# Kernel tuning notes

Hardware: AMD Instinct MI355X
Metric: run time of the kernel (lower is better)

The kernel has to match this reference:

```python
import jax, jax.numpy as jnp
import numpy as np
import math

B, S, E, H = 2, 4096, 1024, 16
W = 256  # one-sided attention window (attention_window // 2)


def setup_inputs() -> dict:
    key = jax.random.key(0)
    ks = jax.random.split(key, 7)
    init = lambda k, shp: jax.random.normal(k, shp, jnp.float32) * 0.02
    return {
        "hidden_states": jax.random.normal(ks[0], (B, S, E), jnp.float32),
        "attention_mask": jnp.zeros((B, S), jnp.int32),  # 0 = local attention
        "q_w": init(ks[1], (E, E)), "q_b": jnp.zeros((E,), jnp.float32),
        "k_w": init(ks[2], (E, E)), "k_b": jnp.zeros((E,), jnp.float32),
        "v_w": init(ks[3], (E, E)), "v_b": jnp.zeros((E,), jnp.float32),
    }


def _banded_attention(hidden_states, attention_mask, q_w, q_b, k_w, k_b, v_w, v_b):
    D = E // H          # head dim
    w = W               # one-sided window
    nc = S // w         # number of query chunks of length w
    # Projections (torch Linear: x @ W.T + b); query pre-scaled by sqrt(head_dim)
    q = (hidden_states @ q_w.T + q_b) / math.sqrt(D)
    k = hidden_states @ k_w.T + k_b
    v = hidden_states @ v_w.T + v_b
    heads = lambda x: x.reshape(B, S, H, D).transpose(0, 2, 1, 3)  # [B,H,S,D]
    q, k, v = heads(q), heads(k), heads(v)

    qc = q.reshape(B, H, nc, w, D)                       # [B,H,nc,w,D]
    pad = lambda x: jnp.pad(x, ((0, 0), (0, 0), (w, w), (0, 0)))
    # chunk c of keys/values covers padded positions [c*w, c*w + 3w)
    idx = (jnp.arange(nc) * w)[:, None] + jnp.arange(3 * w)[None, :]  # [nc,3w]
    kc = pad(k)[:, :, idx]                               # [B,H,nc,3w,D]
    vc = pad(v)[:, :, idx]                               # [B,H,nc,3w,D]

    # banded scores: query x in chunk attends padded key y; rel offset = y-w-x
    scores = jnp.einsum('bhcxd,bhcyd->bhcxy', qc, kc)    # [B,H,nc,w,3w]

    # additive mask from attention_mask (!=0 -> -10000 at that key position)
    fm = jnp.where(attention_mask != 0, -10000.0, 0.0)   # [B,S]
    fmc = jnp.pad(fm, ((0, 0), (w, w)))[:, idx]          # [B,nc,3w]
    scores = scores + fmc[:, None, :, None, :]

    # validity: |rel| <= w (the 2w+1 band) and key index j in [0, S)
    x = jnp.arange(w)[:, None]                           # [w,1]
    y = jnp.arange(3 * w)[None, :]                       # [1,3w]
    rel = y - w - x                                      # [w,3w]
    j = (jnp.arange(nc) * w)[:, None, None] + (y - w)[None]  # [nc,1,3w] key idx
    valid = (jnp.abs(rel) <= w)[None] & (j >= 0) & (j < S)   # [nc,w,3w]
    scores = jnp.where(valid[None, None], scores, -jnp.inf)

    probs = jax.nn.softmax(scores.astype(jnp.float32), axis=-1)
    ctx = jnp.einsum('bhcxy,bhcyd->bhcxd', probs, vc)    # [B,H,nc,w,D]
    return ctx.reshape(B, H, S, D).transpose(0, 2, 1, 3).reshape(B, S, E)


def reference(hidden_states, attention_mask, q_w, q_b, k_w, k_b, v_w, v_b):
    return _banded_attention(hidden_states, attention_mask,
                             q_w, q_b, k_w, k_b, v_w, v_b)
```

## Files before the change

### kernel.cpp

```cpp
#include <hip/hip_runtime.h>
#include <math.h>

constexpr int Bn  = 2;
constexpr int Sn  = 4096;
constexpr int En  = 1024;
constexpr int Hn  = 16;
constexpr int Mtot = Bn * Sn;
constexpr int Kp  = 1024;
constexpr int QT   = 128;
constexpr int NST  = 10;
constexpr int PADK = 68;
constexpr int PADP = 36;

typedef __bf16    bf16x8 __attribute__((ext_vector_type(8)));
typedef __bf16    bf16x4 __attribute__((ext_vector_type(4)));
typedef _Float16  f16x8  __attribute__((ext_vector_type(8)));
typedef _Float16  f16x4  __attribute__((ext_vector_type(4)));
typedef float     f32x4  __attribute__((ext_vector_type(4)));

__global__ void __launch_bounds__(256)
cvt_all_kernel(const float* __restrict__ hs,
               const float* __restrict__ qw, const float* __restrict__ kw,
               const float* __restrict__ vw,
               _Float16* __restrict__ hs16, _Float16* __restrict__ w16)
{
    if (blockIdx.x < 8192) {
        int t = blockIdx.x * 256 + threadIdx.x;
        int m = t >> 8;
        int k = (t & 255) << 2;
        float4 x = *(const float4*)&hs[((size_t)m << 10) + k];
        f16x4 h;
        h[0] = (_Float16)x.x; h[1] = (_Float16)x.y;
        h[2] = (_Float16)x.z; h[3] = (_Float16)x.w;
        *(f16x4*)&hs16[((size_t)m << 10) + k] = h;
    } else {
        int t = (blockIdx.x - 8192) * 256 + threadIdx.x;
        int gn = t >> 8;
        int k  = (t & 255) << 2;
        int p  = gn >> 10, n = gn & 1023;
        const float* src = (p == 0) ? qw : (p == 1) ? kw : vw;
        float4 x = *(const float4*)&src[((size_t)n << 10) + k];
        f16x4 h;
        h[0] = (_Float16)x.x; h[1] = (_Float16)x.y;
        h[2] = (_Float16)x.z; h[3] = (_Float16)x.w;
        *(f16x4*)&w16[((size_t)gn << 10) + k] = h;
    }
}

__device__ inline void load_lds16(const void* g, void* s) {
    __builtin_amdgcn_global_load_lds((const __attribute__((address_space(1))) void*)g,
                                     (__attribute__((address_space(3))) void*)s,
                                     16, 0, 0);
}

__global__ void __launch_bounds__(256)
qkv_mfma_kernel(const _Float16* __restrict__ A2, const _Float16* __restrict__ B2,
                const float* __restrict__ qb, const float* __restrict__ kb,
                const float* __restrict__ vb,
                __bf16* __restrict__ q16, __bf16* __restrict__ k16,
                __bf16* __restrict__ vt16)
{
    __shared__ _Float16 As[128 * 32];
    __shared__ _Float16 Bs[128 * 32];

    const int tid  = threadIdx.x;
    const int m0   = blockIdx.x * 128;
    const int n0   = blockIdx.y * 128;
    const int w    = tid >> 6;
    const int lane = tid & 63;
    const int wm   = w >> 1, wn = w & 1;
    const int mrow = lane & 15, quad = lane >> 4;

    const int stRow = w * 16 + (lane >> 2);
    const int stCol = (lane & 3) * 8;

    f32x4 acc[4][4] = {};

    const _Float16* Abase = A2 + (size_t)(m0 + stRow) * Kp + stCol;
    const _Float16* Bbase = B2 + (size_t)(n0 + stRow) * Kp + stCol;
    _Float16* AsW = &As[w * 512];
    _Float16* BsW = &Bs[w * 512];

    for (int k0 = 0; k0 < Kp; k0 += 32) {
        load_lds16(Abase + k0,            AsW);
        load_lds16(Abase + 64 * Kp + k0,  AsW + 2048);
        load_lds16(Bbase + k0,            BsW);
        load_lds16(Bbase + 64 * Kp + k0,  BsW + 2048);
        __syncthreads();
        f16x8 af[4], bfr[4];
#pragma unroll
        for (int t = 0; t < 4; t++) {
            af[t]  = *(const f16x8*)&As[(wm * 64 + t * 16 + mrow) * 32 + quad * 8];
            bfr[t] = *(const f16x8*)&Bs[(wn * 64 + t * 16 + mrow) * 32 + quad * 8];
        }
#pragma unroll
        for (int ti = 0; ti < 4; ti++)
#pragma unroll
            for (int tj = 0; tj < 4; tj++)
                acc[ti][tj] = __builtin_amdgcn_mfma_f32_16x16x32_f16(
                    af[ti], bfr[tj], acc[ti][tj], 0, 0, 0);
        __syncthreads();
    }

    const int p = n0 >> 10;
    const float* bptr = (p == 0) ? qb : (p == 1) ? kb : vb;
#pragma unroll
    for (int tj = 0; tj < 4; tj++) {
        const int n  = n0 + wn * 64 + tj * 16 + mrow;
        const float bv = bptr[n & 1023];
        const int hh = (n & 1023) >> 6, dd = n & 63;
#pragma unroll
        for (int ti = 0; ti < 4; ti++) {
            const int m  = m0 + wm * 64 + ti * 16 + quad * 4;
            const int bb = m >> 12, ss = m & 4095;
            const size_t bhh = (size_t)(bb * Hn + hh);
            if (p == 0) {
#pragma unroll
                for (int r = 0; r < 4; r++)
                    q16[(bhh * Sn + ss + r) * 64 + dd] =
                        (__bf16)((acc[ti][tj][r] + bv) * 0.125f);
            } else if (p == 1) {
#pragma unroll
                for (int r = 0; r < 4; r++)
                    k16[(bhh * Sn + ss + r) * 64 + dd] =
                        (__bf16)(acc[ti][tj][r] + bv);
            } else {
                bf16x4 pv4;
#pragma unroll
                for (int r = 0; r < 4; r++)
                    pv4[r] = (__bf16)(acc[ti][tj][r] + bv);
                *(bf16x4*)&vt16[(bhh * 64 + dd) * (size_t)Sn + ss] = pv4;
            }
        }
    }
}

__global__ void __launch_bounds__(256, 4)
banded_attn_kernel(const __bf16* __restrict__ q16, const __bf16* __restrict__ k16,
                   const __bf16* __restrict__ vt16, const int* __restrict__ mask,
                   float* __restrict__ out)
{
    __shared__ __bf16 Kt[64 * PADK];
    __shared__ __bf16 Vt[64 * PADK];
    __shared__ __bf16 Pt[4][32 * PADP];
    __shared__ float  Msh[704];

    const int flat = blockIdx.x;
    const int g    = flat & 7;
    const int j    = flat >> 3;
    const int pl   = g * 4 + (j >> 5);
    const int c    = j & 31;
    const int h    = pl & 15;
    const int b    = pl >> 4;

    const int bh = b * Hn + h;
    const int i0 = c * QT;
    const int jwin0 = i0 - 256;
    const int tid  = threadIdx.x;
    const int wv   = tid >> 6;
    const int lane = tid & 63;
    const int quad = lane >> 4, mrow = lane & 15;

#pragma unroll
    for (int rep = 0; rep < 3; rep++) {
        int idx = rep * 256 + tid;
        if (idx < 640) {
            int jg = jwin0 + idx;
            float mv = 0.f;
            if (jg >= 0 && jg < Sn && mask[b * Sn + jg] != 0) mv = -10000.f;
            Msh[idx] = mv;
        }
    }

    bf16x8 qf[2][2];
    const __bf16* qbase = q16 + (((size_t)bh * Sn + i0 + wv * 32) << 6);
#pragma unroll
    for (int tjq = 0; tjq < 2; tjq++)
#pragma unroll
        for (int kc = 0; kc < 2; kc++)
            qf[tjq][kc] = *(const bf16x8*)(qbase + (16 * tjq + mrow) * 64 + 32 * kc + 8 * quad);

    const int sr = lane >> 3;
    const int sc = lane & 7;
    bf16x8 kreg0, kreg1, vreg0, vreg1;
    auto gload = [&](int st) {
        const int j0 = jwin0 + st * 64;
        const int r0 = wv * 16 + sr;
        const int r1 = wv * 16 + 8 + sr;
        int jk0 = j0 + r0; jk0 = jk0 < 0 ? 0 : (jk0 > Sn - 1 ? Sn - 1 : jk0);
        int jk1 = j0 + r1; jk1 = jk1 < 0 ? 0 : (jk1 > Sn - 1 ? Sn - 1 : jk1);
        kreg0 = *(const bf16x8*)&k16[(((size_t)bh * Sn + jk0) << 6) + sc * 8];
        kreg1 = *(const bf16x8*)&k16[(((size_t)bh * Sn + jk1) << 6) + sc * 8];
        int jv = j0 + sc * 8; jv = jv < 0 ? 0 : (jv > Sn - 8 ? Sn - 8 : jv);
        vreg0 = *(const bf16x8*)&vt16[((size_t)bh * 64 + r0) * Sn + jv];
        vreg1 = *(const bf16x8*)&vt16[((size_t)bh * 64 + r1) * Sn + jv];
    };
    auto swrite = [&]() {
        *(bf16x8*)&Kt[(wv * 16 + sr) * PADK + sc * 8]     = kreg0;
        *(bf16x8*)&Kt[(wv * 16 + 8 + sr) * PADK + sc * 8] = kreg1;
        *(bf16x8*)&Vt[(wv * 16 + sr) * PADK + sc * 8]     = vreg0;
        *(bf16x8*)&Vt[(wv * 16 + 8 + sr) * PADK + sc * 8] = vreg1;
    };

    f32x4 acc_o[4][2] = {};
    float lrun[2] = {0.f, 0.f};
    __bf16* Pw = &Pt[wv][0];
    const int stlo = wv >> 1;

    gload(0);
    for (int st = 0; st < NST; st++) {
        __syncthreads();
        swrite();
        __syncthreads();
        if (st + 1 < NST) gload(st + 1);

        const int j0 = jwin0 + 64 * st;
        const bool activ = (st >= stlo) && (st <= stlo + 8) &&
                           (j0 + 63 >= 0) && (j0 < Sn);
        if (activ) {
            const bool fast = (st > stlo) && (st < stlo + 8) &&
                              (j0 >= 0) && (j0 + 63 < Sn);
#pragma unroll
            for (int half = 0; half < 2; half++) {
#pragma unroll
                for (int t2 = 0; t2 < 2; t2++) {
                    const int ti = 2 * half + t2;
                    bf16x8 ak0 = *(const bf16x8*)&Kt[(16 * ti + mrow) * PADK + quad * 8];
                    bf16x8 ak1 = *(const bf16x8*)&Kt[(16 * ti + mrow) * PADK + 32 + quad * 8];
                    const int y0 = 64 * st + 16 * ti + 4 * quad;
                    f32x4 ms4 = *(const f32x4*)&Msh[y0];
#pragma unroll
                    for (int tjq = 0; tjq < 2; tjq++) {
                        f32x4 s = {};
                        s = __builtin_amdgcn_mfma_f32_16x16x32_bf16(ak0, qf[tjq][0], s, 0, 0, 0);
                        s = __builtin_amdgcn_mfma_f32_16x16x32_bf16(ak1, qf[tjq][1], s, 0, 0, 0);
                        bf16x4 pk;
                        float psum = 0.f;
                        if (fast) {
#pragma unroll
                            for (int r = 0; r < 4; r++) {
                                float pv = __expf(s[r] + ms4[r]);
                                psum += pv;
                                pk[r] = (__bf16)pv;
                            }
                        } else {
                            const int xq = 32 * wv + 16 * tjq + mrow;
#pragma unroll
                            for (int r = 0; r < 4; r++) {
                                const int y = y0 + r;
                                bool ok = ((unsigned)(y - xq) <= 512u) &
                                          ((unsigned)(jwin0 + y) < 4096u);
                                float pv = ok ? __expf(s[r] + ms4[r]) : 0.f;
                                psum += pv;
                                pk[r] = (__bf16)pv;
                            }
                        }
                        lrun[tjq] += psum;
                        *(bf16x4*)&Pw[(16 * tjq + mrow) * PADP + 16 * t2 + 4 * quad] = pk;
                    }
                }
                bf16x8 av[4];
#pragma unroll
                for (int dt = 0; dt < 4; dt++)
                    av[dt] = *(const bf16x8*)&Vt[(16 * dt + mrow) * PADK + 32 * half + quad * 8];
#pragma unroll
                for (int tjq = 0; tjq < 2; tjq++) {
                    bf16x8 pf = *(const bf16x8*)&Pw[(16 * tjq + mrow) * PADP + quad * 8];
#pragma unroll
                    for (int dt = 0; dt < 4; dt++)
                        acc_o[dt][tjq] = __builtin_amdgcn_mfma_f32_16x16x32_bf16(
                            av[dt], pf, acc_o[dt][tjq], 0, 0, 0);
                }
            }
        }
    }

    float inv[2];
#pragma unroll
    for (int tjq = 0; tjq < 2; tjq++) {
        float l = lrun[tjq];
        l += __shfl_xor(l, 16);
        l += __shfl_xor(l, 32);
        inv[tjq] = 1.0f / l;
    }
#pragma unroll
    for (int dt = 0; dt < 4; dt++)
#pragma unroll
        for (int tjq = 0; tjq < 2; tjq++) {
            f32x4 o = acc_o[dt][tjq];
            o[0] *= inv[tjq]; o[1] *= inv[tjq]; o[2] *= inv[tjq]; o[3] *= inv[tjq];
            float* dst = out + ((size_t)(b * Sn + i0 + wv * 32 + 16 * tjq + mrow)) * En
                             + h * 64 + 16 * dt + 4 * quad;
            *(f32x4*)dst = o;
        }
}

extern "C" void kernel_launch(void* const* d_in, const int* in_sizes, int n_in,
                              void* d_out, int out_size, void* d_ws, size_t ws_size,
                              hipStream_t stream) {
    const float* hs  = (const float*)d_in[0];
    const int*  mask = (const int*)d_in[1];
    const float* qw  = (const float*)d_in[2];
    const float* qb  = (const float*)d_in[3];
    const float* kw  = (const float*)d_in[4];
    const float* kb  = (const float*)d_in[5];
    const float* vw  = (const float*)d_in[6];
    const float* vb  = (const float*)d_in[7];
    float* out = (float*)d_out;

    _Float16* hs16 = (_Float16*)d_ws;
    _Float16* w16  = (_Float16*)((char*)d_ws + (size_t)16777216);
    __bf16*   q16  = (__bf16*)((char*)d_ws + (size_t)23068672);
    __bf16*   k16  = (__bf16*)((char*)d_ws + (size_t)39845888);
    __bf16*   vt16 = (__bf16*)((char*)d_ws + (size_t)56623104);

    cvt_all_kernel<<<11264, 256, 0, stream>>>(hs, qw, kw, vw, hs16, w16);

    dim3 pgrid(Mtot / 128, 3072 / 128);
    qkv_mfma_kernel<<<pgrid, 256, 0, stream>>>(hs16, w16, qb, kb, vb, q16, k16, vt16);

    banded_attn_kernel<<<1024, 256, 0, stream>>>(q16, k16, vt16, mask, out);
}
```

Baseline: 223.0 us.

## Load K/V fragments directly from global memory, dropping shared-memory staging

The attention kernel no longer stages 64-row K and V tiles through LDS with per-stage barriers and a register prefetch. Each wave now reads its MFMA K and V^T operands straight from global memory (relying on L1/L2 for reuse across waves), and a single barrier after the mask load replaces the two per-iteration syncs. This removes the block-wide synchronization and lets waves skip inactive stages independently. In exchange, each wave issues redundant global loads and gives up explicit latency hiding from the prefetch.

```diff
diff --git a/kernel.cpp b/kernel.cpp
--- a/kernel.cpp
+++ b/kernel.cpp
@@ -9,7 +9,6 @@
 constexpr int Kp  = 1024;
 constexpr int QT   = 128;
 constexpr int NST  = 10;
-constexpr int PADK = 68;
 constexpr int PADP = 36;
 
 typedef __bf16    bf16x8 __attribute__((ext_vector_type(8)));
@@ -140,8 +139,6 @@
                    const __bf16* __restrict__ vt16, const int* __restrict__ mask,
                    float* __restrict__ out)
 {
-    __shared__ __bf16 Kt[64 * PADK];
-    __shared__ __bf16 Vt[64 * PADK];
     __shared__ __bf16 Pt[4][32 * PADP];
     __shared__ float  Msh[704];
 
@@ -171,6 +168,7 @@
             Msh[idx] = mv;
         }
     }
+    __syncthreads();
 
     bf16x8 qf[2][2];
     const __bf16* qbase = q16 + (((size_t)bh * Sn + i0 + wv * 32) << 6);
@@ -180,97 +178,74 @@
         for (int kc = 0; kc < 2; kc++)
             qf[tjq][kc] = *(const bf16x8*)(qbase + (16 * tjq + mrow) * 64 + 32 * kc + 8 * quad);
 
-    const int sr = lane >> 3;
-    const int sc = lane & 7;
-    bf16x8 kreg0, kreg1, vreg0, vreg1;
-    auto gload = [&](int st) {
-        const int j0 = jwin0 + st * 64;
-        const int r0 = wv * 16 + sr;
-        const int r1 = wv * 16 + 8 + sr;
-        int jk0 = j0 + r0; jk0 = jk0 < 0 ? 0 : (jk0 > Sn - 1 ? Sn - 1 : jk0);
-        int jk1 = j0 + r1; jk1 = jk1 < 0 ? 0 : (jk1 > Sn - 1 ? Sn - 1 : jk1);
-        kreg0 = *(const bf16x8*)&k16[(((size_t)bh * Sn + jk0) << 6) + sc * 8];
-        kreg1 = *(const bf16x8*)&k16[(((size_t)bh * Sn + jk1) << 6) + sc * 8];
-        int jv = j0 + sc * 8; jv = jv < 0 ? 0 : (jv > Sn - 8 ? Sn - 8 : jv);
-        vreg0 = *(const bf16x8*)&vt16[((size_t)bh * 64 + r0) * Sn + jv];
-        vreg1 = *(const bf16x8*)&vt16[((size_t)bh * 64 + r1) * Sn + jv];
-    };
-    auto swrite = [&]() {
-        *(bf16x8*)&Kt[(wv * 16 + sr) * PADK + sc * 8]     = kreg0;
-        *(bf16x8*)&Kt[(wv * 16 + 8 + sr) * PADK + sc * 8] = kreg1;
-        *(bf16x8*)&Vt[(wv * 16 + sr) * PADK + sc * 8]     = vreg0;
-        *(bf16x8*)&Vt[(wv * 16 + 8 + sr) * PADK + sc * 8] = vreg1;
-    };
+    const __bf16* kbase = k16 + ((size_t)bh * Sn << 6);
+    const __bf16* vbase = vt16 + (size_t)bh * 64 * (size_t)Sn;
 
     f32x4 acc_o[4][2] = {};
     float lrun[2] = {0.f, 0.f};
     __bf16* Pw = &Pt[wv][0];
     const int stlo = wv >> 1;
 
-    gload(0);
     for (int st = 0; st < NST; st++) {
-        __syncthreads();
-        swrite();
-        __syncthreads();
-        if (st + 1 < NST) gload(st + 1);
-
         const int j0 = jwin0 + 64 * st;
-        const bool activ = (st >= stlo) && (st <= stlo + 8) &&
-                           (j0 + 63 >= 0) && (j0 < Sn);
-        if (activ) {
-            const bool fast = (st > stlo) && (st < stlo + 8) &&
-                              (j0 >= 0) && (j0 + 63 < Sn);
-#pragma unroll
-            for (int half = 0; half < 2; half++) {
-#pragma unroll
-                for (int t2 = 0; t2 < 2; t2++) {
-                    const int ti = 2 * half + t2;
-                    bf16x8 ak0 = *(const bf16x8*)&Kt[(16 * ti + mrow) * PADK + quad * 8];
-                    bf16x8 ak1 = *(const bf16x8*)&Kt[(16 * ti + mrow) * PADK + 32 + quad * 8];
-                    const int y0 = 64 * st + 16 * ti + 4 * quad;
-                    f32x4 ms4 = *(const f32x4*)&Msh[y0];
-#pragma unroll
-                    for (int tjq = 0; tjq < 2; tjq++) {
-                        f32x4 s = {};
-                        s = __builtin_amdgcn_mfma_f32_16x16x32_bf16(ak0, qf[tjq][0], s, 0, 0, 0);
-                        s = __builtin_amdgcn_mfma_f32_16x16x32_bf16(ak1, qf[tjq][1], s, 0, 0, 0);
-                        bf16x4 pk;
-                        float psum = 0.f;
-                        if (fast) {
-#pragma unroll
-                            for (int r = 0; r < 4; r++) {
-                                float pv = __expf(s[r] + ms4[r]);
-                                psum += pv;
-                                pk[r] = (__bf16)pv;
-                            }
-                        } else {
-                            const int xq = 32 * wv + 16 * tjq + mrow;
-#pragma unroll
-                            for (int r = 0; r < 4; r++) {
-                                const int y = y0 + r;
-                                bool ok = ((unsigned)(y - xq) <= 512u) &
-                                          ((unsigned)(jwin0 + y) < 4096u);
-                                float pv = ok ? __expf(s[r] + ms4[r]) : 0.f;
-                                psum += pv;
-                                pk[r] = (__bf16)pv;
-                            }
+        if (st < stlo || st > stlo + 8 || j0 + 63 < 0 || j0 >= Sn) continue;
+        const bool fast = (st > stlo) && (st < stlo + 8) &&
+                          (j0 >= 0) && (j0 + 63 < Sn);
+#pragma unroll
+        for (int half = 0; half < 2; half++) {
+#pragma unroll
+            for (int t2 = 0; t2 < 2; t2++) {
+                const int ti = 2 * half + t2;
+                int jr = j0 + 16 * ti + mrow;
+                jr = jr < 0 ? 0 : (jr > Sn - 1 ? Sn - 1 : jr);
+                const __bf16* krow = kbase + ((size_t)jr << 6);
+                bf16x8 ak0 = *(const bf16x8*)(krow + 8 * quad);
+                bf16x8 ak1 = *(const bf16x8*)(krow + 32 + 8 * quad);
+                const int y0 = 64 * st + 16 * ti + 4 * quad;
+                f32x4 ms4 = *(const f32x4*)&Msh[y0];
+#pragma unroll
+                for (int tjq = 0; tjq < 2; tjq++) {
+                    f32x4 s = {};
+                    s = __builtin_amdgcn_mfma_f32_16x16x32_bf16(ak0, qf[tjq][0], s, 0, 0, 0);
+                    s = __builtin_amdgcn_mfma_f32_16x16x32_bf16(ak1, qf[tjq][1], s, 0, 0, 0);
+                    bf16x4 pk;
+                    float psum = 0.f;
+                    if (fast) {
+#pragma unroll
+                        for (int r = 0; r < 4; r++) {
+                            float pv = __expf(s[r] + ms4[r]);
+                            psum += pv;
+                            pk[r] = (__bf16)pv;
                         }
-                        lrun[tjq] += psum;
-                        *(bf16x4*)&Pw[(16 * tjq + mrow) * PADP + 16 * t2 + 4 * quad] = pk;
+                    } else {
+                        const int xq = 32 * wv + 16 * tjq + mrow;
+#pragma unroll
+                        for (int r = 0; r < 4; r++) {
+                            const int y = y0 + r;
+                            bool ok = ((unsigned)(y - xq) <= 512u) &
+                                      ((unsigned)(jwin0 + y) < 4096u);
+                            float pv = ok ? __expf(s[r] + ms4[r]) : 0.f;
+                            psum += pv;
+                            pk[r] = (__bf16)pv;
+                        }
                     }
+                    lrun[tjq] += psum;
+                    *(bf16x4*)&Pw[(16 * tjq + mrow) * PADP + 16 * t2 + 4 * quad] = pk;
                 }
-                bf16x8 av[4];
+            }
+            int vcol = j0 + 32 * half + 8 * quad;
+            vcol = vcol < 0 ? 0 : (vcol > Sn - 8 ? Sn - 8 : vcol);
+            bf16x8 av[4];
+#pragma unroll
+            for (int dt = 0; dt < 4; dt++)
+                av[dt] = *(const bf16x8*)(vbase + (size_t)(16 * dt + mrow) * Sn + vcol);
+#pragma unroll
+            for (int tjq = 0; tjq < 2; tjq++) {
+                bf16x8 pf = *(const bf16x8*)&Pw[(16 * tjq + mrow) * PADP + quad * 8];
 #pragma unroll
                 for (int dt = 0; dt < 4; dt++)
-                    av[dt] = *(const bf16x8*)&Vt[(16 * dt + mrow) * PADK + 32 * half + quad * 8];
-#pragma unroll
-                for (int tjq = 0; tjq < 2; tjq++) {
-                    bf16x8 pf = *(const bf16x8*)&Pw[(16 * tjq + mrow) * PADP + quad * 8];
-#pragma unroll
-                    for (int dt = 0; dt < 4; dt++)
-                        acc_o[dt][tjq] = __builtin_amdgcn_mfma_f32_16x16x32_bf16(
-                            av[dt], pf, acc_o[dt][tjq], 0, 0, 0);
-                }
+                    acc_o[dt][tjq] = __builtin_amdgcn_mfma_f32_16x16x32_bf16(
+                        av[dt], pf, acc_o[dt][tjq], 0, 0, 0);
             }
         }
     }
```

After: 237.9 us. 6.7% more time.
